# Performance work log

Measured on AMD Instinct MI355X. Metric: run time of the kernel, lower is better.

The kernel has to match this reference:

```python
import jax, jax.numpy as jnp
import numpy as np

ENCODER_DIM, HIDDEN_DIM, ATT_DIM = 2048, 1024, 1024
B, P = 128, 196  # batch, num_pixels


def setup_inputs() -> dict:
    key = jax.random.key(0)
    ks = jax.random.split(key, 8)
    s_e = 1.0 / np.sqrt(ENCODER_DIM)
    s_h = 1.0 / np.sqrt(HIDDEN_DIM)
    s_a = 1.0 / np.sqrt(ATT_DIM)
    return {
        "encoder_out": jax.random.normal(ks[0], (B, P, ENCODER_DIM), jnp.float32),
        "decoder_hidden": jax.random.normal(ks[1], (B, HIDDEN_DIM), jnp.float32),
        # nn.Linear params (weight is [out, in] in torch; store transposed for x @ W)
        "W_enc": jax.random.uniform(ks[2], (ENCODER_DIM, ATT_DIM), jnp.float32, -s_e, s_e),
        "b_enc": jax.random.uniform(ks[3], (ATT_DIM,), jnp.float32, -s_e, s_e),
        "W_dec": jax.random.uniform(ks[4], (HIDDEN_DIM, ATT_DIM), jnp.float32, -s_h, s_h),
        "b_dec": jax.random.uniform(ks[5], (ATT_DIM,), jnp.float32, -s_h, s_h),
        "W_full": jax.random.uniform(ks[6], (ATT_DIM,), jnp.float32, -s_a, s_a),
        "b_full": jax.random.uniform(ks[7], (), jnp.float32, -s_a, s_a),
    }


def reference(encoder_out, decoder_hidden, W_enc, b_enc, W_dec, b_dec, W_full, b_full):
    # att1: [B, P, A]; att2: [B, 1, A]
    att1 = jnp.einsum("bpe,ea->bpa", encoder_out, W_enc) + b_enc
    att2 = decoder_hidden @ W_dec + b_dec
    att = jax.nn.relu(att1 + att2[:, None, :])
    scores = jnp.einsum("bpa,a->bp", att, W_full) + b_full  # [B, P]
    alpha = jax.nn.softmax(scores, axis=1)
    context = jnp.einsum("bpe,bp->be", encoder_out, alpha)  # [B, E]
    return (context, alpha)
```

## Files before the change

kernel.cpp:

```cpp
#include <hip/hip_runtime.h>
#include <hip/hip_bf16.h>


#define B_   128
#define P_   196
#define E_   2048
#define H_   1024
#define A_   1024
#define M_   (B_ * P_)
#define NKSTEP (E_ / 64)

typedef __bf16 bf16x8 __attribute__((ext_vector_type(8)));
typedef float f32x4 __attribute__((ext_vector_type(4)));

__device__ __bf16 g_wt[(size_t)A_ * E_];
__device__ __bf16 g_enc[(size_t)M_ * E_];

__device__ __forceinline__ bf16x8 cvt8r(const float4 a, const float4 b) {
    bf16x8 r;
    r[0] = (__bf16)a.x; r[1] = (__bf16)a.y; r[2] = (__bf16)a.z; r[3] = (__bf16)a.w;
    r[4] = (__bf16)b.x; r[5] = (__bf16)b.y; r[6] = (__bf16)b.z; r[7] = (__bf16)b.w;
    return r;
}

__device__ __forceinline__ void gl16(const void* g, void* l) {
    __builtin_amdgcn_global_load_lds(
        (const __attribute__((address_space(1))) unsigned int*)g,
        (__attribute__((address_space(3))) unsigned int*)l, 16, 0, 0);
}

__global__ __launch_bounds__(256) void k_cvt(const float* __restrict__ enc) {
    const size_t n = (size_t)M_ * E_;
    const size_t stride = (size_t)gridDim.x * 256 * 8;
    for (size_t i = ((size_t)blockIdx.x * 256 + threadIdx.x) * 8; i < n;
         i += stride) {
        const float4 a = *(const float4*)(enc + i);
        const float4 b = *(const float4*)(enc + i + 4);
        *(bf16x8*)&g_enc[i] = cvt8r(a, b);
    }
}

__global__ __launch_bounds__(256) void k_wt(const float* __restrict__ w) {
    __shared__ __bf16 tile[64][72];
    const int t = threadIdx.x;
    const int a0 = blockIdx.x * 64, e0 = blockIdx.y * 64;
    const int er = t >> 2, c0 = (t & 3) * 16;
#pragma unroll
    for (int j = 0; j < 4; ++j) {
        const float4 v =
            *(const float4*)&w[(size_t)(e0 + er) * A_ + a0 + c0 + j * 4];
        tile[c0 + j * 4 + 0][er] = (__bf16)v.x;
        tile[c0 + j * 4 + 1][er] = (__bf16)v.y;
        tile[c0 + j * 4 + 2][er] = (__bf16)v.z;
        tile[c0 + j * 4 + 3][er] = (__bf16)v.w;
    }
    __syncthreads();
    const int ar = t >> 2, es0 = (t & 3) * 16;
    *(bf16x8*)&g_wt[(size_t)(a0 + ar) * E_ + e0 + es0] =
        *(const bf16x8*)&tile[ar][es0];
    *(bf16x8*)&g_wt[(size_t)(a0 + ar) * E_ + e0 + es0 + 8] =
        *(const bf16x8*)&tile[ar][es0 + 8];
}

__global__ __launch_bounds__(256) void k_att2(
    const float* __restrict__ dh, const float* __restrict__ wdec,
    const float* __restrict__ benc, const float* __restrict__ bdec,
    float* __restrict__ scores, float* __restrict__ att2p) {
    const int t = threadIdx.x;
    const int a0 = blockIdx.x * 128;
    const int b0 = blockIdx.y * 8;
    const int bid = blockIdx.y * 8 + blockIdx.x;
    const int gi = bid * 256 + t;
    if (gi < M_) scores[gi] = 0.f;
    __shared__ float hs[8][H_];
    __shared__ float red[256][8];
    for (int i = t; i < 8 * H_; i += 256)
        hs[i >> 10][i & 1023] = dh[(size_t)(b0 + (i >> 10)) * H_ + (i & 1023)];
    __syncthreads();
    const int a = a0 + (t & 127);
    const int h0 = (t >> 7) * 512;
    float acc[8] = {};
#pragma unroll 4
    for (int h = 0; h < 512; ++h) {
        const float w = wdec[(size_t)(h0 + h) * A_ + a];
#pragma unroll
        for (int j = 0; j < 8; ++j) acc[j] += hs[j][h0 + h] * w;
    }
#pragma unroll
    for (int j = 0; j < 8; ++j) red[t][j] = acc[j];
    __syncthreads();
    if (t < 128) {
        const float bb = benc[a0 + t] + bdec[a0 + t];
#pragma unroll
        for (int j = 0; j < 8; ++j)
            att2p[(size_t)(b0 + j) * A_ + a0 + t] =
                red[t][j] + red[t + 128][j] + bb;
    }
}

__global__ __launch_bounds__(256, 2) void k_gemm_scores(
    const float* __restrict__ att2p,
    const float* __restrict__ wfull,
    float* __restrict__ scores) {
    __shared__ __align__(16) __bf16 As[2][128 * 64];
    __shared__ __align__(16) __bf16 Bs[2][128 * 64];
    __shared__ float red[2][128];

    const int t = threadIdx.x;
    const int lane = t & 63;
    const int wave = t >> 6;
    const int wm = wave >> 1, wn = wave & 1;
    const int q = lane >> 4, r = lane & 15;
    const int orig = blockIdx.y * 8 + blockIdx.x;
    const int L = (orig & 7) * (M_ / 128) + (orig >> 3);
    const int bn = L & 7, bm = L >> 3;
    const int m0 = bm * 128, n0 = bn * 128;

    const int rbase = wave * 8 + (lane >> 3);
    const int cx = ((t & 7) ^ ((t >> 3) & 7)) * 16;
    const char* pa = (const char*)g_enc + (size_t)(m0 + rbase) * 4096 + cx;
    const char* pb = (const char*)g_wt  + (size_t)(n0 + rbase) * 4096 + cx;
    char* ad0 = (char*)&As[0][0] + wave * 1024;
    char* ad1 = (char*)&As[1][0] + wave * 1024;
    char* bd0 = (char*)&Bs[0][0] + wave * 1024;
    char* bd1 = (char*)&Bs[1][0] + wave * 1024;

    f32x4 acc[4][4] = {};

#pragma unroll
    for (int i = 0; i < 4; ++i)
        gl16(pa + (size_t)i * 131072, ad0 + i * 4096);
#pragma unroll
    for (int i = 0; i < 4; ++i)
        gl16(pb + (size_t)i * 131072, bd0 + i * 4096);

    int cur = 0;
    for (int kt = 0; kt < NKSTEP; ++kt) {
        asm volatile("s_waitcnt vmcnt(0)" ::: "memory");
        asm volatile("s_waitcnt lgkmcnt(0)" ::: "memory");
        __builtin_amdgcn_s_barrier();

        const char* AsC = (const char*)&As[cur][0];
        const char* BsC = (const char*)&Bs[cur][0];

        if (kt + 1 < NKSTEP) {
            char* ad = cur ? ad0 : ad1;
            char* bd = cur ? bd0 : bd1;
            const size_t ko = (size_t)(kt + 1) * 128;
#pragma unroll
            for (int i = 0; i < 4; ++i)
                gl16(pa + (size_t)i * 131072 + ko, ad + i * 4096);
#pragma unroll
            for (int i = 0; i < 4; ++i)
                gl16(pb + (size_t)i * 131072 + ko, bd + i * 4096);
        }

#pragma unroll
        for (int ks = 0; ks < 2; ++ks) {
            bf16x8 af[4], bfv[4];
#pragma unroll
            for (int f = 0; f < 4; ++f) {
                const int mf = wm * 64 + f * 16 + r;
                af[f] = *(const bf16x8*)(AsC + mf * 128 +
                        ((ks * 64 + q * 16) ^ ((r & 7) << 4)));
            }
#pragma unroll
            for (int f = 0; f < 4; ++f) {
                const int nf = wn * 64 + f * 16 + r;
                bfv[f] = *(const bf16x8*)(BsC + nf * 128 +
                        ((ks * 64 + q * 16) ^ ((r & 7) << 4)));
            }
#pragma unroll
            for (int fm = 0; fm < 4; ++fm)
#pragma unroll
                for (int fn = 0; fn < 4; ++fn)
                    acc[fm][fn] = __builtin_amdgcn_mfma_f32_16x16x32_bf16(
                        af[fm], bfv[fn], acc[fm][fn], 0, 0, 0);
        }
        cur ^= 1;
    }

    float psum[4][4];
    const float* wfb = wfull + n0 + wn * 64;
#pragma unroll
    for (int fm = 0; fm < 4; ++fm) {
#pragma unroll
        for (int i = 0; i < 4; ++i) {
            const int row_g = m0 + wm * 64 + fm * 16 + q * 4 + i;
            const unsigned bidx = (unsigned)row_g / 196u;
            const float* a2 = att2p + (size_t)bidx * A_ + n0 + wn * 64;
            float s = 0.f;
#pragma unroll
            for (int fn = 0; fn < 4; ++fn) {
                const int cl = fn * 16 + r;
                float v = acc[fm][fn][i] + a2[cl];
                v = fmaxf(v, 0.f);
                s += v * wfb[cl];
            }
            psum[fm][i] = s;
        }
    }
#pragma unroll
    for (int fm = 0; fm < 4; ++fm)
#pragma unroll
        for (int i = 0; i < 4; ++i) {
            float v = psum[fm][i];
            v += __shfl_xor(v, 1);
            v += __shfl_xor(v, 2);
            v += __shfl_xor(v, 4);
            v += __shfl_xor(v, 8);
            if (r == 0) red[wn][wm * 64 + fm * 16 + q * 4 + i] = v;
        }
    __syncthreads();
    if (t < 128) atomicAdd(&scores[m0 + t], red[0][t] + red[1][t]);
}

__global__ __launch_bounds__(256) void k_softmax(
    const float* __restrict__ scores, float* __restrict__ out) {
    const int b = blockIdx.x;
    const int t = threadIdx.x;
    __shared__ float sm[256];
    const bool act = t < P_;
    const float val = act ? scores[b * P_ + t] : 0.f;
    sm[t] = act ? val : -1e30f;
    __syncthreads();
    for (int off = 128; off > 0; off >>= 1) {
        if (t < off) sm[t] = fmaxf(sm[t], sm[t + off]);
        __syncthreads();
    }
    const float mx = sm[0];
    __syncthreads();
    const float e = act ? __expf(val - mx) : 0.f;
    sm[t] = e;
    __syncthreads();
    for (int off = 128; off > 0; off >>= 1) {
        if (t < off) sm[t] = sm[t] + sm[t + off];
        __syncthreads();
    }
    const float inv = 1.0f / sm[0];
    if (act) out[(size_t)B_ * E_ + b * P_ + t] = e * inv;
}

__global__ __launch_bounds__(256) void k_context(
    const float* __restrict__ enc, float* __restrict__ out) {
    const int b = blockIdx.y;
    const int e0 = blockIdx.x * 1024 + threadIdx.x * 4;
    __shared__ float al[P_];
    if (threadIdx.x < P_)
        al[threadIdx.x] = out[(size_t)B_ * E_ + b * P_ + threadIdx.x];
    __syncthreads();
    float ax = 0.f, ay = 0.f, az = 0.f, aw = 0.f;
    const float* base = enc + (size_t)b * P_ * E_ + e0;
#pragma unroll 14
    for (int p = 0; p < P_; ++p) {
        const float4 v = *(const float4*)(base + (size_t)p * E_);
        const float ap = al[p];
        ax += ap * v.x; ay += ap * v.y; az += ap * v.z; aw += ap * v.w;
    }
    float4 sv; sv.x = ax; sv.y = ay; sv.z = az; sv.w = aw;
    *(float4*)(out + (size_t)b * E_ + e0) = sv;
}

extern "C" void kernel_launch(void* const* d_in, const int* in_sizes, int n_in,
                              void* d_out, int out_size, void* d_ws,
                              size_t ws_size, hipStream_t stream) {
    const float* enc   = (const float*)d_in[0];
    const float* dh    = (const float*)d_in[1];
    const float* wenc  = (const float*)d_in[2];
    const float* benc  = (const float*)d_in[3];
    const float* wdec  = (const float*)d_in[4];
    const float* bdec  = (const float*)d_in[5];
    const float* wfull = (const float*)d_in[6];
    float* out = (float*)d_out;

    float* att2p  = out;
    float* scores = (float*)((char*)d_out + 524288);

    k_cvt<<<2048, 256, 0, stream>>>(enc);
    k_wt<<<dim3(A_ / 64, E_ / 64), 256, 0, stream>>>(wenc);
    k_att2<<<dim3(8, 16), 256, 0, stream>>>(dh, wdec, benc, bdec, scores,
                                            att2p);
    k_gemm_scores<<<dim3(8, M_ / 128), 256, 0, stream>>>(att2p, wfull,
                                                         scores);
    k_softmax<<<B_, 256, 0, stream>>>(scores, out);
    k_context<<<dim3(2, B_), 256, 0, stream>>>(enc, out);
}
```

Measured before the change: 595.4 us.

## Merge preprocessing kernels into one launch and read bf16 encoder in context

Combines the encoder fp32-to-bf16 conversion, the W_enc transpose and the att2 projection into a single kernel, with block ranges assigned to each job, so they share one launch and run concurrently. The context kernel now reads the bf16 encoder copy instead of the fp32 input, halving the bytes it streams. The cost is lower precision in the context output, since it is built from bf16-rounded encoder values, and each block in the fused kernel reserves the larger shared-memory footprint.

```diff
diff --git a/kernel.cpp b/kernel.cpp
--- a/kernel.cpp
+++ b/kernel.cpp
@@ -29,72 +29,79 @@
         (__attribute__((address_space(3))) unsigned int*)l, 16, 0, 0);
 }
 
-__global__ __launch_bounds__(256) void k_cvt(const float* __restrict__ enc) {
-    const size_t n = (size_t)M_ * E_;
-    const size_t stride = (size_t)gridDim.x * 256 * 8;
-    for (size_t i = ((size_t)blockIdx.x * 256 + threadIdx.x) * 8; i < n;
-         i += stride) {
-        const float4 a = *(const float4*)(enc + i);
-        const float4 b = *(const float4*)(enc + i + 4);
-        *(bf16x8*)&g_enc[i] = cvt8r(a, b);
-    }
-}
-
-__global__ __launch_bounds__(256) void k_wt(const float* __restrict__ w) {
-    __shared__ __bf16 tile[64][72];
-    const int t = threadIdx.x;
-    const int a0 = blockIdx.x * 64, e0 = blockIdx.y * 64;
-    const int er = t >> 2, c0 = (t & 3) * 16;
-#pragma unroll
-    for (int j = 0; j < 4; ++j) {
-        const float4 v =
-            *(const float4*)&w[(size_t)(e0 + er) * A_ + a0 + c0 + j * 4];
-        tile[c0 + j * 4 + 0][er] = (__bf16)v.x;
-        tile[c0 + j * 4 + 1][er] = (__bf16)v.y;
-        tile[c0 + j * 4 + 2][er] = (__bf16)v.z;
-        tile[c0 + j * 4 + 3][er] = (__bf16)v.w;
-    }
-    __syncthreads();
-    const int ar = t >> 2, es0 = (t & 3) * 16;
-    *(bf16x8*)&g_wt[(size_t)(a0 + ar) * E_ + e0 + es0] =
-        *(const bf16x8*)&tile[ar][es0];
-    *(bf16x8*)&g_wt[(size_t)(a0 + ar) * E_ + e0 + es0 + 8] =
-        *(const bf16x8*)&tile[ar][es0 + 8];
-}
-
-__global__ __launch_bounds__(256) void k_att2(
+__global__ __launch_bounds__(256) void k_pre(
+    const float* __restrict__ enc, const float* __restrict__ w,
     const float* __restrict__ dh, const float* __restrict__ wdec,
     const float* __restrict__ benc, const float* __restrict__ bdec,
     float* __restrict__ scores, float* __restrict__ att2p) {
+    __shared__ float smem[10240];
+    const int bid = blockIdx.x;
     const int t = threadIdx.x;
-    const int a0 = blockIdx.x * 128;
-    const int b0 = blockIdx.y * 8;
-    const int bid = blockIdx.y * 8 + blockIdx.x;
-    const int gi = bid * 256 + t;
-    if (gi < M_) scores[gi] = 0.f;
-    __shared__ float hs[8][H_];
-    __shared__ float red[256][8];
-    for (int i = t; i < 8 * H_; i += 256)
-        hs[i >> 10][i & 1023] = dh[(size_t)(b0 + (i >> 10)) * H_ + (i & 1023)];
-    __syncthreads();
-    const int a = a0 + (t & 127);
-    const int h0 = (t >> 7) * 512;
-    float acc[8] = {};
+
+    if (bid < 1792) {
+        size_t i = ((size_t)bid * 256 + t) * 8;
+        const size_t stride = (size_t)1792 * 256 * 8;
+#pragma unroll
+        for (int it = 0; it < 14; ++it, i += stride) {
+            const float4 a = *(const float4*)(enc + i);
+            const float4 b = *(const float4*)(enc + i + 4);
+            *(bf16x8*)&g_enc[i] = cvt8r(a, b);
+        }
+    } else if (bid < 1920) {
+        __bf16* tile = (__bf16*)smem;
+        const int er = t >> 2, c0 = (t & 3) * 16;
+        const int ar = t >> 2, es0 = (t & 3) * 16;
+#pragma unroll 1
+        for (int j = 0; j < 4; ++j) {
+            const int job = (bid - 1792) * 4 + j;
+            const int a0 = (job & 15) * 64, e0 = (job >> 4) * 64;
+            __syncthreads();
+#pragma unroll
+            for (int jj = 0; jj < 4; ++jj) {
+                const float4 v = *(const float4*)&w[(size_t)(e0 + er) * A_ +
+                                                    a0 + c0 + jj * 4];
+                tile[(c0 + jj * 4 + 0) * 72 + er] = (__bf16)v.x;
+                tile[(c0 + jj * 4 + 1) * 72 + er] = (__bf16)v.y;
+                tile[(c0 + jj * 4 + 2) * 72 + er] = (__bf16)v.z;
+                tile[(c0 + jj * 4 + 3) * 72 + er] = (__bf16)v.w;
+            }
+            __syncthreads();
+            *(bf16x8*)&g_wt[(size_t)(a0 + ar) * E_ + e0 + es0] =
+                *(const bf16x8*)&tile[ar * 72 + es0];
+            *(bf16x8*)&g_wt[(size_t)(a0 + ar) * E_ + e0 + es0 + 8] =
+                *(const bf16x8*)&tile[ar * 72 + es0 + 8];
+        }
+    } else {
+        const int vbid = bid - 1920;
+        const int a0 = (vbid & 7) * 128;
+        const int b0 = (vbid >> 3) * 8;
+        const int gi = vbid * 256 + t;
+        if (gi < M_) scores[gi] = 0.f;
+        float (*hs)[H_] = (float (*)[H_])smem;
+        float (*red)[8] = (float (*)[8])(smem + 8192);
+        for (int i = t; i < 8 * H_; i += 256)
+            hs[i >> 10][i & 1023] =
+                dh[(size_t)(b0 + (i >> 10)) * H_ + (i & 1023)];
+        __syncthreads();
+        const int a = a0 + (t & 127);
+        const int h0 = (t >> 7) * 512;
+        float acc[8] = {};
 #pragma unroll 4
-    for (int h = 0; h < 512; ++h) {
-        const float w = wdec[(size_t)(h0 + h) * A_ + a];
-#pragma unroll
-        for (int j = 0; j < 8; ++j) acc[j] += hs[j][h0 + h] * w;
-    }
-#pragma unroll
-    for (int j = 0; j < 8; ++j) red[t][j] = acc[j];
-    __syncthreads();
-    if (t < 128) {
-        const float bb = benc[a0 + t] + bdec[a0 + t];
-#pragma unroll
-        for (int j = 0; j < 8; ++j)
-            att2p[(size_t)(b0 + j) * A_ + a0 + t] =
-                red[t][j] + red[t + 128][j] + bb;
+        for (int h = 0; h < 512; ++h) {
+            const float wv = wdec[(size_t)(h0 + h) * A_ + a];
+#pragma unroll
+            for (int j = 0; j < 8; ++j) acc[j] += hs[j][h0 + h] * wv;
+        }
+#pragma unroll
+        for (int j = 0; j < 8; ++j) red[t][j] = acc[j];
+        __syncthreads();
+        if (t < 128) {
+            const float bb = benc[a0 + t] + bdec[a0 + t];
+#pragma unroll
+            for (int j = 0; j < 8; ++j)
+                att2p[(size_t)(b0 + j) * A_ + a0 + t] =
+                    red[t][j] + red[t + 128][j] + bb;
+        }
     }
 }
 
@@ -241,24 +248,25 @@
     if (act) out[(size_t)B_ * E_ + b * P_ + t] = e * inv;
 }
 
-__global__ __launch_bounds__(256) void k_context(
-    const float* __restrict__ enc, float* __restrict__ out) {
+__global__ __launch_bounds__(256) void k_context(float* __restrict__ out) {
     const int b = blockIdx.y;
-    const int e0 = blockIdx.x * 1024 + threadIdx.x * 4;
+    const int e0 = blockIdx.x * 512 + threadIdx.x * 2;
     __shared__ float al[P_];
     if (threadIdx.x < P_)
         al[threadIdx.x] = out[(size_t)B_ * E_ + b * P_ + threadIdx.x];
     __syncthreads();
-    float ax = 0.f, ay = 0.f, az = 0.f, aw = 0.f;
-    const float* base = enc + (size_t)b * P_ * E_ + e0;
+    float ax = 0.f, ay = 0.f;
+    const char* base = (const char*)g_enc +
+                       ((size_t)b * P_) * (E_ * 2) + (size_t)e0 * 2;
 #pragma unroll 14
     for (int p = 0; p < P_; ++p) {
-        const float4 v = *(const float4*)(base + (size_t)p * E_);
+        const unsigned u = *(const unsigned*)(base + (size_t)p * (E_ * 2));
         const float ap = al[p];
-        ax += ap * v.x; ay += ap * v.y; az += ap * v.z; aw += ap * v.w;
-    }
-    float4 sv; sv.x = ax; sv.y = ay; sv.z = az; sv.w = aw;
-    *(float4*)(out + (size_t)b * E_ + e0) = sv;
+        ax += ap * __uint_as_float(u << 16);
+        ay += ap * __uint_as_float(u & 0xffff0000u);
+    }
+    float2 sv; sv.x = ax; sv.y = ay;
+    *(float2*)(out + (size_t)b * E_ + e0) = sv;
 }
 
 extern "C" void kernel_launch(void* const* d_in, const int* in_sizes, int n_in,
@@ -276,12 +284,10 @@
     float* att2p  = out;
     float* scores = (float*)((char*)d_out + 524288);
 
-    k_cvt<<<2048, 256, 0, stream>>>(enc);
-    k_wt<<<dim3(A_ / 64, E_ / 64), 256, 0, stream>>>(wenc);
-    k_att2<<<dim3(8, 16), 256, 0, stream>>>(dh, wdec, benc, bdec, scores,
-                                            att2p);
+    k_pre<<<2048, 256, 0, stream>>>(enc, wenc, dh, wdec, benc, bdec, scores,
+                                    att2p);
     k_gemm_scores<<<dim3(8, M_ / 128), 256, 0, stream>>>(att2p, wfull,
                                                          scores);
     k_softmax<<<B_, 256, 0, stream>>>(scores, out);
-    k_context<<<dim3(2, B_), 256, 0, stream>>>(enc, out);
-}
+    k_context<<<dim3(4, 128), 256, 0, stream>>>(out);
+}
```

Measured after the change: 567.0 us. 4.8% less time.
